# Kernel tuning notes

Measured on AMD Instinct MI355X. Metric: run time of the kernel, lower is better.

Reference implementation:

```python
import jax, jax.numpy as jnp
import numpy as np
import math

ALPHA = 1.0  # surrogate-gradient sharpness, self.alpha() == 1.0

@jax.custom_vjp
def spike(x):
    # Heaviside forward (PiecewiseQuadratic.apply forward)
    return (x >= 0).astype(x.dtype)

def _spike_fwd(x):
    return spike(x), x

def _spike_bwd(x, g):
    # piecewise-quadratic surrogate: g'(x) = alpha - alpha^2*|x| for |x| < 1/alpha, else 0
    sg = jnp.where(jnp.abs(x) < 1.0 / ALPHA, -(ALPHA ** 2) * jnp.abs(x) + ALPHA, 0.0)
    return (g * sg.astype(x.dtype),)

spike.defvjp(_spike_fwd, _spike_bwd)


def setup_inputs() -> dict:
    key = jax.random.key(0)
    kx = jax.random.fold_in(key, 0)
    B, T, N = 64, 64, 8192
    x = jax.random.normal(kx, (B, T, N), dtype=jnp.float32)
    # parameters per __init__: tau=2.0 -> stored param log(1/(tau-1)) = 0.0
    tau_p = jnp.array([math.log(1.0 / (2.0 - 1.0))], dtype=jnp.float32)
    lamb = jnp.array([0.2], dtype=jnp.float32)
    th = jnp.array([1.0], dtype=jnp.float32)  # non-learnable
    return {"x": x, "tau_p": tau_p, "lamb": lamb, "th": th}


def reference(x, tau_p, lamb, th):
    sig = jax.nn.sigmoid(tau_p)  # scalar leak factor, shape [1]
    xt = jnp.swapaxes(x, 0, 1)   # [T, B, N] for scan over time

    def step(last, x_t):
        u = last * sig + x_t
        s = spike(u - th)
        new_last = (u + lamb * (u - last)) * (1.0 - s)  # momentum + hard reset
        return new_last, s

    last0 = jnp.zeros_like(x[:, 0])
    _, out = jax.lax.scan(step, last0, xt)  # out: [T, B, N]
    return jnp.swapaxes(out, 0, 1)         # [B, T, N]
```

## Files before the change

kernel.cpp:

```cpp
#include <hip/hip_runtime.h>


#define LIF_B 64
#define LIF_T 64
#define LIF_N 8192
#define NV2 (LIF_N / 2)
#define UN 8
#define NSTAGE (LIF_T / UN)

typedef float f2 __attribute__((ext_vector_type(2)));

__global__ __launch_bounds__(256, 4) void lif_fwd_kernel(
    const f2* __restrict__ x,
    const float* __restrict__ tau_p,
    const float* __restrict__ lamb_p,
    const float* __restrict__ th_p,
    f2* __restrict__ out)
{
    const int tid = blockIdx.x * blockDim.x + threadIdx.x;
    const int b   = tid >> 12;
    const int n2  = tid & (NV2 - 1);

    const float sig  = 1.0f / (1.0f + expf(-tau_p[0]));
    const float lamb = lamb_p[0];
    const float th   = th_p[0];

    float lx = 0.0f, ly = 0.0f;
    const size_t base = (size_t)b * LIF_T * NV2 + n2;

    f2 cur[UN], nxt[UN];
    unsigned int bits[4] = {0u, 0u, 0u, 0u};

#pragma unroll
    for (int i = 0; i < UN; ++i)
        cur[i] = x[base + (size_t)i * NV2];

#pragma unroll
    for (int k = 0; k < NSTAGE; ++k) {
        if (k + 1 < NSTAGE) {
#pragma unroll
            for (int i = 0; i < UN; ++i)
                nxt[i] = x[base + (size_t)((k + 1) * UN + i) * NV2];
        }

#pragma unroll
        for (int i = 0; i < UN; ++i) {
            const int t = k * UN + i;
            f2 v = cur[i];
            {
                float u = __fadd_rn(__fmul_rn(lx, sig), v.x);
                bool  c = (u >= th);
                float s = c ? 1.0f : 0.0f;
                lx = __fmul_rn(__fadd_rn(u, __fmul_rn(lamb, __fsub_rn(u, lx))),
                               __fsub_rn(1.0f, s));
                bits[t >> 4] |= c ? (1u << ((t & 15) * 2)) : 0u;
            }
            {
                float u = __fadd_rn(__fmul_rn(ly, sig), v.y);
                bool  c = (u >= th);
                float s = c ? 1.0f : 0.0f;
                ly = __fmul_rn(__fadd_rn(u, __fmul_rn(lamb, __fsub_rn(u, ly))),
                               __fsub_rn(1.0f, s));
                bits[t >> 4] |= c ? (1u << ((t & 15) * 2 + 1)) : 0u;
            }
        }

#pragma unroll
        for (int i = 0; i < UN; ++i)
            cur[i] = nxt[i];
    }

#pragma unroll
    for (int t = 0; t < LIF_T; ++t) {
        const unsigned int w = bits[t >> 4];
        f2 sv;
        sv.x = ((w >> ((t & 15) * 2))     & 1u) ? 1.0f : 0.0f;
        sv.y = ((w >> ((t & 15) * 2 + 1)) & 1u) ? 1.0f : 0.0f;
        __builtin_nontemporal_store(sv, &out[base + (size_t)t * NV2]);
    }
}

extern "C" void kernel_launch(void* const* d_in, const int* in_sizes, int n_in,
                              void* d_out, int out_size, void* d_ws, size_t ws_size,
                              hipStream_t stream) {
    (void)in_sizes; (void)n_in; (void)out_size; (void)d_ws; (void)ws_size;

    const f2*    x     = (const f2*)d_in[0];
    const float* tau_p = (const float*)d_in[1];
    const float* lamb  = (const float*)d_in[2];
    const float* th    = (const float*)d_in[3];
    f2*          out   = (f2*)d_out;

    const int total_threads = LIF_B * NV2;
    const int block = 256;
    const int grid  = total_threads / block;
    lif_fwd_kernel<<<grid, block, 0, stream>>>(x, tau_p, lamb, th, out);
}
```

Before: 235.9 us.

## Split LIF into byte-spike compute kernel plus vectorized expand kernel

When a large enough workspace is available, the scan now writes one byte per spike to the workspace. A second kernel then expands those bytes into float outputs with contiguous 16-byte nontemporal stores. This targets the cost of the strided 8-byte float stores in the time-major scan. The price is extra workspace traffic and a second launch. The fallback fused kernel now stores spikes inside the time loop instead of packing bits.

```diff
diff --git a/kernel.cpp b/kernel.cpp
--- a/kernel.cpp
+++ b/kernel.cpp
@@ -7,10 +7,94 @@
 #define NV2 (LIF_N / 2)
 #define UN 8
 #define NSTAGE (LIF_T / UN)
+#define WS_BYTES ((size_t)LIF_B * LIF_T * LIF_N)
 
 typedef float f2 __attribute__((ext_vector_type(2)));
+typedef float f4 __attribute__((ext_vector_type(4)));
+typedef unsigned char u8;
+typedef unsigned int  u32;
+typedef u8 uc2 __attribute__((ext_vector_type(2)));
 
-__global__ __launch_bounds__(256, 4) void lif_fwd_kernel(
+__global__ __launch_bounds__(256) void lif_compute_kernel(
+    const f2* __restrict__ x,
+    const float* __restrict__ tau_p,
+    const float* __restrict__ lamb_p,
+    const float* __restrict__ th_p,
+    uc2* __restrict__ spk)
+{
+    const int tid = blockIdx.x * blockDim.x + threadIdx.x;
+    const int b   = tid >> 12;
+    const int n2  = tid & (NV2 - 1);
+
+    const float sig  = 1.0f / (1.0f + expf(-tau_p[0]));
+    const float lamb = lamb_p[0];
+    const float th   = th_p[0];
+
+    float lx = 0.0f, ly = 0.0f;
+    const size_t base = (size_t)b * LIF_T * NV2 + n2;
+
+    f2 cur[UN], nxt[UN];
+
+#pragma unroll
+    for (int i = 0; i < UN; ++i)
+        cur[i] = x[base + (size_t)i * NV2];
+
+#pragma unroll
+    for (int k = 0; k < NSTAGE; ++k) {
+        if (k + 1 < NSTAGE) {
+#pragma unroll
+            for (int i = 0; i < UN; ++i)
+                nxt[i] = x[base + (size_t)((k + 1) * UN + i) * NV2];
+        }
+
+#pragma unroll
+        for (int i = 0; i < UN; ++i) {
+            f2 v = cur[i];
+            uc2 sb;
+            {
+                float u = __fadd_rn(__fmul_rn(lx, sig), v.x);
+                bool  c = (u >= th);
+                float s = c ? 1.0f : 0.0f;
+                lx = __fmul_rn(__fadd_rn(u, __fmul_rn(lamb, __fsub_rn(u, lx))),
+                               __fsub_rn(1.0f, s));
+                sb.x = c ? (u8)1 : (u8)0;
+            }
+            {
+                float u = __fadd_rn(__fmul_rn(ly, sig), v.y);
+                bool  c = (u >= th);
+                float s = c ? 1.0f : 0.0f;
+                ly = __fmul_rn(__fadd_rn(u, __fmul_rn(lamb, __fsub_rn(u, ly))),
+                               __fsub_rn(1.0f, s));
+                sb.y = c ? (u8)1 : (u8)0;
+            }
+            spk[base + (size_t)(k * UN + i) * NV2] = sb;
+        }
+
+#pragma unroll
+        for (int i = 0; i < UN; ++i)
+            cur[i] = nxt[i];
+    }
+}
+
+__global__ __launch_bounds__(256) void lif_expand_kernel(
+    const u32* __restrict__ spk,
+    f4* __restrict__ out)
+{
+    const int base = blockIdx.x * (256 * 16) + threadIdx.x;
+#pragma unroll
+    for (int i = 0; i < 16; ++i) {
+        const int idx = base + i * 256;
+        const u32 w = spk[idx];
+        f4 v;
+        v.x = (w & 0x000000ffu) ? 1.0f : 0.0f;
+        v.y = (w & 0x0000ff00u) ? 1.0f : 0.0f;
+        v.z = (w & 0x00ff0000u) ? 1.0f : 0.0f;
+        v.w = (w & 0xff000000u) ? 1.0f : 0.0f;
+        __builtin_nontemporal_store(v, &out[idx]);
+    }
+}
+
+__global__ __launch_bounds__(256, 4) void lif_fused_kernel(
     const f2* __restrict__ x,
     const float* __restrict__ tau_p,
     const float* __restrict__ lamb_p,
@@ -29,8 +113,6 @@
     const size_t base = (size_t)b * LIF_T * NV2 + n2;
 
     f2 cur[UN], nxt[UN];
-    unsigned int bits[4] = {0u, 0u, 0u, 0u};
-
 #pragma unroll
     for (int i = 0; i < UN; ++i)
         cur[i] = x[base + (size_t)i * NV2];
@@ -42,57 +124,49 @@
             for (int i = 0; i < UN; ++i)
                 nxt[i] = x[base + (size_t)((k + 1) * UN + i) * NV2];
         }
-
 #pragma unroll
         for (int i = 0; i < UN; ++i) {
-            const int t = k * UN + i;
             f2 v = cur[i];
+            f2 sv;
             {
                 float u = __fadd_rn(__fmul_rn(lx, sig), v.x);
-                bool  c = (u >= th);
-                float s = c ? 1.0f : 0.0f;
+                float s = (u >= th) ? 1.0f : 0.0f;
                 lx = __fmul_rn(__fadd_rn(u, __fmul_rn(lamb, __fsub_rn(u, lx))),
                                __fsub_rn(1.0f, s));
-                bits[t >> 4] |= c ? (1u << ((t & 15) * 2)) : 0u;
+                sv.x = s;
             }
             {
                 float u = __fadd_rn(__fmul_rn(ly, sig), v.y);
-                bool  c = (u >= th);
-                float s = c ? 1.0f : 0.0f;
+                float s = (u >= th) ? 1.0f : 0.0f;
                 ly = __fmul_rn(__fadd_rn(u, __fmul_rn(lamb, __fsub_rn(u, ly))),
                                __fsub_rn(1.0f, s));
-                bits[t >> 4] |= c ? (1u << ((t & 15) * 2 + 1)) : 0u;
+                sv.y = s;
             }
+            __builtin_nontemporal_store(sv, &out[base + (size_t)(k * UN + i) * NV2]);
         }
-
 #pragma unroll
         for (int i = 0; i < UN; ++i)
             cur[i] = nxt[i];
-    }
-
-#pragma unroll
-    for (int t = 0; t < LIF_T; ++t) {
-        const unsigned int w = bits[t >> 4];
-        f2 sv;
-        sv.x = ((w >> ((t & 15) * 2))     & 1u) ? 1.0f : 0.0f;
-        sv.y = ((w >> ((t & 15) * 2 + 1)) & 1u) ? 1.0f : 0.0f;
-        __builtin_nontemporal_store(sv, &out[base + (size_t)t * NV2]);
     }
 }
 
 extern "C" void kernel_launch(void* const* d_in, const int* in_sizes, int n_in,
                               void* d_out, int out_size, void* d_ws, size_t ws_size,
                               hipStream_t stream) {
-    (void)in_sizes; (void)n_in; (void)out_size; (void)d_ws; (void)ws_size;
+    (void)in_sizes; (void)n_in; (void)out_size;
 
     const f2*    x     = (const f2*)d_in[0];
     const float* tau_p = (const float*)d_in[1];
     const float* lamb  = (const float*)d_in[2];
     const float* th    = (const float*)d_in[3];
-    f2*          out   = (f2*)d_out;
 
-    const int total_threads = LIF_B * NV2;
-    const int block = 256;
-    const int grid  = total_threads / block;
-    lif_fwd_kernel<<<grid, block, 0, stream>>>(x, tau_p, lamb, th, out);
+    if (d_ws != nullptr && ws_size >= WS_BYTES) {
+        lif_compute_kernel<<<1024, 256, 0, stream>>>(
+            x, tau_p, lamb, th, (uc2*)d_ws);
+        lif_expand_kernel<<<2048, 256, 0, stream>>>(
+            (const u32*)d_ws, (f4*)d_out);
+    } else {
+        lif_fused_kernel<<<1024, 256, 0, stream>>>(
+            x, tau_p, lamb, th, (f2*)d_out);
+    }
 }
```

Measured after the change: 241.7 us. +2.5%, slower.
